# Kernel optimization log

Hardware: AMD Instinct MI355X
Metric: run time of the kernel (lower is better)

## Reference

```python
import jax, jax.numpy as jnp
import numpy as np

EPS = 1e-5  # nn.BatchNorm2d default eps
K = 3       # number of adjacency subsets


def setup_inputs() -> dict:
    key = jax.random.key(0)
    ks = jax.random.split(key, 8)
    N, C, T, V = 64, 64, 256, 25
    Cout = 64
    x = jax.random.normal(ks[0], (N, C, T, V), dtype=jnp.float32)
    A = jax.random.uniform(ks[1], (K, V, V), dtype=jnp.float32) * 0.1  # normalized-ish adjacency
    PA = jnp.ones((K, V, V), dtype=jnp.float32)  # torch.ones_like(A) init
    Wc = jax.random.normal(ks[2], (K * Cout, C), dtype=jnp.float32) * 0.05  # 1x1 conv weight
    bc = jax.random.normal(ks[3], (K * Cout,), dtype=jnp.float32) * 0.01
    gamma = 0.5 + jax.random.uniform(ks[4], (Cout,), dtype=jnp.float32)
    beta = jax.random.normal(ks[5], (Cout,), dtype=jnp.float32) * 0.1
    mean = jax.random.normal(ks[6], (Cout,), dtype=jnp.float32) * 0.1
    var = 0.5 + jax.random.uniform(ks[7], (Cout,), dtype=jnp.float32)
    return {"x": x, "A": A, "PA": PA, "Wc": Wc, "bc": bc,
            "gamma": gamma, "beta": beta, "mean": mean, "var": var}


def reference(x, A, PA, Wc, bc, gamma, beta, mean, var):
    # x: (n, c, t, v). in_channels == out_channels -> residual is identity.
    n, c, t, v = x.shape
    res = x
    Aeff = A * PA  # (k, v, w)
    # 1x1 conv: (n,c,t,v) x (o,c) -> (n,o,t,v), o = K*Cout
    y = jnp.einsum('nctv,oc->notv', x, Wc) + bc[None, :, None, None]
    cout = y.shape[1] // K
    y = y.reshape(n, K, cout, t, v)
    # per-subset graph aggregation: (n,k,c,t,v) x (k,v,w) -> (n,c,t,w)
    z = jnp.einsum('nkctv,kvw->nctw', y, Aeff)
    # BatchNorm2d (eval mode) over channel dim
    inv = jax.lax.rsqrt(var + EPS)
    bn = (z - mean[None, :, None, None]) * (gamma * inv)[None, :, None, None] + beta[None, :, None, None]
    return jax.nn.relu(bn + res)
```

## Files before the change

### kernel.cpp

```cpp
#include <hip/hip_runtime.h>
#include <hip/hip_bf16.h>

typedef __attribute__((ext_vector_type(8))) short short8;
typedef __attribute__((ext_vector_type(4))) float floatx4;

#define TT 8
#define XS_PITCH 264
#define KCP 200

__device__ __forceinline__ float bf2f(unsigned short u) {
    unsigned int xx = ((unsigned int)u) << 16;
    return __uint_as_float(xx);
}
__device__ __forceinline__ unsigned short f2bf(float f) {
    unsigned int xx = __float_as_uint(f);
    unsigned int r = (xx + 0x7fffu + ((xx >> 16) & 1u)) >> 16;
    return (unsigned short)r;
}

__global__ __launch_bounds__(512) void gcn_fused(
    const float* __restrict__ x,  const float* __restrict__ A,
    const float* __restrict__ PA, const float* __restrict__ Wc,
    const float* __restrict__ bc, const float* __restrict__ gamma_,
    const float* __restrict__ beta_, const float* __restrict__ mean_,
    const float* __restrict__ var_, float* __restrict__ out)
{
#if defined(__gfx950__)
    __shared__ __align__(16) unsigned short Xs[64 * XS_PITCH];
    __shared__ __align__(16) unsigned short AsL[96 * 32];
    __shared__ __align__(16) unsigned short XAs[32 * KCP];
    __shared__ float colsumL[96];
    __shared__ float sL[64], b2L[64], bcL[192];

    const int tid = threadIdx.x;
    const int n  = blockIdx.x >> 5;
    const int t0 = (blockIdx.x & 31) * TT;

    const float* xn = x + (size_t)n * 64 * 256 * 25;
    for (int idx = tid; idx < 64 * TT * 32; idx += 512) {
        int c = idx >> 8, r = idx & 255;
        int t = r >> 5, v = r & 31;
        float val = 0.f;
        if (v < 25) val = xn[(c * 256 + t0 + t) * 25 + v];
        Xs[c * XS_PITCH + r] = f2bf(val);
    }
    for (int idx = tid; idx < 96 * 32; idx += 512) {
        int kw = idx >> 5, v = idx & 31;
        int k = kw >> 5, w = kw & 31;
        unsigned short val = 0;
        if (w < 25 && v < 25) {
            int ai = (k * 25 + v) * 25 + w;
            val = f2bf(A[ai] * PA[ai]);
        }
        AsL[kw * 32 + v] = val;
    }
    if (tid < 96) {
        int k = tid >> 5, w = tid & 31;
        float s = 0.f;
        if (w < 25)
            for (int v = 0; v < 25; ++v) {
                int ai = (k * 25 + v) * 25 + w;
                s += A[ai] * PA[ai];
            }
        colsumL[tid] = s;
    }
    if (tid < 64) {
        float sc = gamma_[tid] * rsqrtf(var_[tid] + 1e-5f);
        sL[tid]  = sc;
        b2L[tid] = beta_[tid] - mean_[tid] * sc;
    }
    if (tid < 192) bcL[tid] = bc[tid];
    __syncthreads();

    const int wave = tid >> 6, lane = tid & 63;
    const int l15 = lane & 15, quad = lane >> 4;

    const int ntA = wave & 3, wmA = wave >> 2;
    short8 aA[3];
#pragma unroll
    for (int ii = 0; ii < 3; ++ii) {
        int mt = wmA + 2 * ii;
        aA[ii] = *(const short8*)&AsL[(mt * 16 + l15) * 32 + quad * 8];
    }

    const int cot = wave & 3, wt = wave >> 2;
    union U8 { short8 v; unsigned short s[8]; };
    short8 wf[6];
#pragma unroll
    for (int ks = 0; ks < 6; ++ks) {
        int k = ks >> 1;
        int co = cot * 16 + l15;
        int cpart = (ks & 1) * 32 + quad * 8;
        const float* wp = &Wc[(k * 64 + co) * 64 + cpart];
        U8 u;
#pragma unroll
        for (int j = 0; j < 8; ++j) u.s[j] = f2bf(wp[j]);
        wf[ks] = u.v;
    }

    for (int t = 0; t < TT; ++t) {
        short8 xb = *(const short8*)&Xs[(ntA * 16 + l15) * XS_PITCH + t * 32 + quad * 8];
        floatx4 fr[3];
#pragma unroll
        for (int ii = 0; ii < 3; ++ii) {
            floatx4 z0 = {0.f, 0.f, 0.f, 0.f};
            fr[ii] = __builtin_amdgcn_mfma_f32_16x16x32_bf16(aA[ii], xb, z0, 0, 0, 0);
        }
        __syncthreads();
#pragma unroll
        for (int ii = 0; ii < 3; ++ii) {
            int mt = wmA + 2 * ii;
#pragma unroll
            for (int r = 0; r < 4; ++r) {
                int kw = mt * 16 + quad * 4 + r;
                int w = kw & 31, k = kw >> 5;
                XAs[w * KCP + k * 64 + ntA * 16 + l15] = f2bf(fr[ii][r]);
            }
        }
        __syncthreads();

        floatx4 zacc = {0.f, 0.f, 0.f, 0.f};
        const unsigned short* xr = &XAs[(wt * 16 + l15) * KCP];
#pragma unroll
        for (int ks = 0; ks < 6; ++ks) {
            short8 bfr = *(const short8*)&xr[ks * 32 + quad * 8];
            zacc = __builtin_amdgcn_mfma_f32_16x16x32_bf16(wf[ks], bfr, zacc, 0, 0, 0);
        }

        int w = wt * 16 + l15;
        if (w < 25) {
            float cs0 = colsumL[w], cs1 = colsumL[32 + w], cs2 = colsumL[64 + w];
#pragma unroll
            for (int r = 0; r < 4; ++r) {
                int co = cot * 16 + quad * 4 + r;
                float bterm = bcL[co] * cs0 + bcL[64 + co] * cs1 + bcL[128 + co] * cs2;
                float xres = bf2f(Xs[co * XS_PITCH + t * 32 + w]);
                float val = sL[co] * (zacc[r] + bterm) + b2L[co] + xres;
                out[((size_t)(n * 64 + co) * 256 + t0 + t) * 25 + w] = fmaxf(val, 0.f);
            }
        }
    }
#else
    (void)x; (void)A; (void)PA; (void)Wc; (void)bc;
    (void)gamma_; (void)beta_; (void)mean_; (void)var_; (void)out;
#endif
}

extern "C" void kernel_launch(void* const* d_in, const int* in_sizes, int n_in,
                              void* d_out, int out_size, void* d_ws, size_t ws_size,
                              hipStream_t stream) {
    (void)in_sizes; (void)n_in; (void)d_ws; (void)ws_size; (void)out_size;
    gcn_fused<<<dim3(64 * 32), dim3(512), 0, stream>>>(
        (const float*)d_in[0],
        (const float*)d_in[1],
        (const float*)d_in[2],
        (const float*)d_in[3],
        (const float*)d_in[4],
        (const float*)d_in[5],
        (const float*)d_in[6],
        (const float*)d_in[7],
        (const float*)d_in[8],
        (float*)d_out);
}
```

Before: 304.8 us.

## Vectorize global loads/stores via LDS staging and double-buffer aggregation scratch

The input tile is now loaded with float4 reads of the contiguous (t,v) span per channel, with the v-padding zero-filled separately. Outputs are kept in registers across all time steps, staged transposed in LDS, and written back as coalesced float4 stores instead of scattered scalar stores. The intermediate XA buffer is double-buffered so one barrier per time step can be dropped. Adjacency fragments are built directly from global memory instead of through LDS, and occupancy is hinted with launch_bounds(512,4), which raises register pressure from the held output values.

```diff
diff --git a/kernel.cpp b/kernel.cpp
--- a/kernel.cpp
+++ b/kernel.cpp
@@ -1,5 +1,4 @@
 #include <hip/hip_runtime.h>
-#include <hip/hip_bf16.h>
 
 typedef __attribute__((ext_vector_type(8))) short short8;
 typedef __attribute__((ext_vector_type(4))) float floatx4;
@@ -7,6 +6,8 @@
 #define TT 8
 #define XS_PITCH 264
 #define KCP 200
+
+#define SMEM_BYTES 61056
 
 __device__ __forceinline__ float bf2f(unsigned short u) {
     unsigned int xx = ((unsigned int)u) << 16;
@@ -18,7 +19,7 @@
     return (unsigned short)r;
 }
 
-__global__ __launch_bounds__(512) void gcn_fused(
+__global__ __launch_bounds__(512, 4) void gcn_fused(
     const float* __restrict__ x,  const float* __restrict__ A,
     const float* __restrict__ PA, const float* __restrict__ Wc,
     const float* __restrict__ bc, const float* __restrict__ gamma_,
@@ -26,33 +27,36 @@
     const float* __restrict__ var_, float* __restrict__ out)
 {
 #if defined(__gfx950__)
-    __shared__ __align__(16) unsigned short Xs[64 * XS_PITCH];
-    __shared__ __align__(16) unsigned short AsL[96 * 32];
-    __shared__ __align__(16) unsigned short XAs[32 * KCP];
-    __shared__ float colsumL[96];
-    __shared__ float sL[64], b2L[64], bcL[192];
+    __shared__ __align__(16) unsigned char smem[SMEM_BYTES];
+    unsigned short* Xs  = (unsigned short*)smem;
+    unsigned short* XA0 = (unsigned short*)(smem + 33792);
+    unsigned short* XA1 = (unsigned short*)(smem + 46592);
+    float* colsumL = (float*)(smem + 59392);
+    float* sL      = (float*)(smem + 59776);
+    float* b2L     = (float*)(smem + 60032);
+    float* bcL     = (float*)(smem + 60288);
+    float* OutT    = (float*)smem;
 
     const int tid = threadIdx.x;
     const int n  = blockIdx.x >> 5;
     const int t0 = (blockIdx.x & 31) * TT;
 
-    const float* xn = x + (size_t)n * 64 * 256 * 25;
-    for (int idx = tid; idx < 64 * TT * 32; idx += 512) {
-        int c = idx >> 8, r = idx & 255;
-        int t = r >> 5, v = r & 31;
-        float val = 0.f;
-        if (v < 25) val = xn[(c * 256 + t0 + t) * 25 + v];
-        Xs[c * XS_PITCH + r] = f2bf(val);
-    }
-    for (int idx = tid; idx < 96 * 32; idx += 512) {
-        int kw = idx >> 5, v = idx & 31;
-        int k = kw >> 5, w = kw & 31;
-        unsigned short val = 0;
-        if (w < 25 && v < 25) {
-            int ai = (k * 25 + v) * 25 + w;
-            val = f2bf(A[ai] * PA[ai]);
-        }
-        AsL[kw * 32 + v] = val;
+    const float* xblk = x + (size_t)n * 409600 + t0 * 25;
+    for (int idx = tid; idx < 3200; idx += 512) {
+        int c = idx / 50, j4 = idx - c * 50;
+        float4 val = *(const float4*)(xblk + c * 6400 + j4 * 4);
+        int flat = j4 * 4;
+#pragma unroll
+        for (int e = 0; e < 4; ++e) {
+            int f = flat + e;
+            int t = f / 25, v = f - t * 25;
+            Xs[c * XS_PITCH + t * 32 + v] = f2bf(((const float*)&val)[e]);
+        }
+    }
+    for (int idx = tid; idx < 64 * TT * 7; idx += 512) {
+        int c = idx / 56, r = idx - c * 56;
+        int t = r / 7, v = 25 + (r - t * 7);
+        Xs[c * XS_PITCH + t * 32 + v] = 0;
     }
     if (tid < 96) {
         int k = tid >> 5, w = tid & 31;
@@ -70,21 +74,33 @@
         b2L[tid] = beta_[tid] - mean_[tid] * sc;
     }
     if (tid < 192) bcL[tid] = bc[tid];
-    __syncthreads();
 
     const int wave = tid >> 6, lane = tid & 63;
     const int l15 = lane & 15, quad = lane >> 4;
 
     const int ntA = wave & 3, wmA = wave >> 2;
+    union U8 { short8 v; unsigned short s[8]; };
     short8 aA[3];
 #pragma unroll
     for (int ii = 0; ii < 3; ++ii) {
         int mt = wmA + 2 * ii;
-        aA[ii] = *(const short8*)&AsL[(mt * 16 + l15) * 32 + quad * 8];
+        int kw = mt * 16 + l15;
+        int k = kw >> 5, w = kw & 31;
+        U8 u;
+#pragma unroll
+        for (int j = 0; j < 8; ++j) {
+            int v2 = quad * 8 + j;
+            float a = 0.f;
+            if (w < 25 && v2 < 25) {
+                int ai = (k * 25 + v2) * 25 + w;
+                a = A[ai] * PA[ai];
+            }
+            u.s[j] = f2bf(a);
+        }
+        aA[ii] = u.v;
     }
 
     const int cot = wave & 3, wt = wave >> 2;
-    union U8 { short8 v; unsigned short s[8]; };
     short8 wf[6];
 #pragma unroll
     for (int ks = 0; ks < 6; ++ks) {
@@ -98,7 +114,14 @@
         wf[ks] = u.v;
     }
 
+    __syncthreads();
+
+    const int w = wt * 16 + l15;
+    float vals[TT][4];
+
+#pragma unroll
     for (int t = 0; t < TT; ++t) {
+        unsigned short* XAw = (t & 1) ? XA1 : XA0;
         short8 xb = *(const short8*)&Xs[(ntA * 16 + l15) * XS_PITCH + t * 32 + quad * 8];
         floatx4 fr[3];
 #pragma unroll
@@ -106,39 +129,53 @@
             floatx4 z0 = {0.f, 0.f, 0.f, 0.f};
             fr[ii] = __builtin_amdgcn_mfma_f32_16x16x32_bf16(aA[ii], xb, z0, 0, 0, 0);
         }
-        __syncthreads();
 #pragma unroll
         for (int ii = 0; ii < 3; ++ii) {
             int mt = wmA + 2 * ii;
 #pragma unroll
             for (int r = 0; r < 4; ++r) {
                 int kw = mt * 16 + quad * 4 + r;
-                int w = kw & 31, k = kw >> 5;
-                XAs[w * KCP + k * 64 + ntA * 16 + l15] = f2bf(fr[ii][r]);
+                int ww = kw & 31, k = kw >> 5;
+                XAw[ww * KCP + k * 64 + ntA * 16 + l15] = f2bf(fr[ii][r]);
             }
         }
         __syncthreads();
 
         floatx4 zacc = {0.f, 0.f, 0.f, 0.f};
-        const unsigned short* xr = &XAs[(wt * 16 + l15) * KCP];
+        const unsigned short* xr = &XAw[(wt * 16 + l15) * KCP];
 #pragma unroll
         for (int ks = 0; ks < 6; ++ks) {
             short8 bfr = *(const short8*)&xr[ks * 32 + quad * 8];
             zacc = __builtin_amdgcn_mfma_f32_16x16x32_bf16(wf[ks], bfr, zacc, 0, 0, 0);
         }
 
-        int w = wt * 16 + l15;
-        if (w < 25) {
-            float cs0 = colsumL[w], cs1 = colsumL[32 + w], cs2 = colsumL[64 + w];
+        float cs0 = colsumL[w], cs1 = colsumL[32 + w], cs2 = colsumL[64 + w];
+#pragma unroll
+        for (int r = 0; r < 4; ++r) {
+            int co = cot * 16 + quad * 4 + r;
+            float bterm = bcL[co] * cs0 + bcL[64 + co] * cs1 + bcL[128 + co] * cs2;
+            float xres = bf2f(Xs[co * XS_PITCH + t * 32 + w]);
+            vals[t][r] = fmaxf(sL[co] * (zacc[r] + bterm) + b2L[co] + xres, 0.f);
+        }
+    }
+
+    __syncthreads();
+    if (w < 25) {
+#pragma unroll
+        for (int t = 0; t < TT; ++t)
 #pragma unroll
             for (int r = 0; r < 4; ++r) {
                 int co = cot * 16 + quad * 4 + r;
-                float bterm = bcL[co] * cs0 + bcL[64 + co] * cs1 + bcL[128 + co] * cs2;
-                float xres = bf2f(Xs[co * XS_PITCH + t * 32 + w]);
-                float val = sL[co] * (zacc[r] + bterm) + b2L[co] + xres;
-                out[((size_t)(n * 64 + co) * 256 + t0 + t) * 25 + w] = fmaxf(val, 0.f);
-            }
-        }
+                OutT[co * 200 + t * 25 + w] = vals[t][r];
+            }
+    }
+    __syncthreads();
+
+    float* oblk = out + (size_t)n * 409600 + t0 * 25;
+    for (int idx = tid; idx < 3200; idx += 512) {
+        int co = idx / 50, j4 = idx - co * 50;
+        float4 vv = *(const float4*)&OutT[co * 200 + j4 * 4];
+        *(float4*)(oblk + co * 6400 + j4 * 4) = vv;
     }
 #else
     (void)x; (void)A; (void)PA; (void)Wc; (void)bc;
```

After: 411.8 us. 35.1% more time.

## Shrink time tile to two steps per block and parallelize waves across them

Applied to the files above, without the earlier changes.

Each block now handles 2 time steps instead of 8, giving 4x more blocks. The wave-to-tile mapping is reorganized so all 8 waves work on both steps at once using a double-buffered XA region, which removes the per-step sync loop. LDS per block drops, so more blocks can be resident per CU, and the column sums are now taken from the bf16-rounded A in shared memory. The trade-off is that A/PA/W/BN setup is redone per block 4x more often, and each row's global load covers only 50 contiguous floats.

```diff
diff --git a/kernel.cpp b/kernel.cpp
--- a/kernel.cpp
+++ b/kernel.cpp
@@ -1,11 +1,10 @@
 #include <hip/hip_runtime.h>
-#include <hip/hip_bf16.h>
 
 typedef __attribute__((ext_vector_type(8))) short short8;
 typedef __attribute__((ext_vector_type(4))) float floatx4;
 
-#define TT 8
-#define XS_PITCH 264
+#define XSP 72
+#define ASP 32
 #define KCP 200
 
 __device__ __forceinline__ float bf2f(unsigned short u) {
@@ -26,43 +25,40 @@
     const float* __restrict__ var_, float* __restrict__ out)
 {
 #if defined(__gfx950__)
-    __shared__ __align__(16) unsigned short Xs[64 * XS_PITCH];
-    __shared__ __align__(16) unsigned short AsL[96 * 32];
-    __shared__ __align__(16) unsigned short XAs[32 * KCP];
+    __shared__ __align__(16) unsigned short Xs[64 * XSP];
+    __shared__ __align__(16) unsigned short AsL[96 * ASP];
+    __shared__ __align__(16) unsigned short XA[2 * 32 * KCP];
     __shared__ float colsumL[96];
     __shared__ float sL[64], b2L[64], bcL[192];
 
-    const int tid = threadIdx.x;
-    const int n  = blockIdx.x >> 5;
-    const int t0 = (blockIdx.x & 31) * TT;
+    const int tid  = threadIdx.x;
+    const int n    = blockIdx.x >> 7;
+    const int t0   = (blockIdx.x & 127) * 2;
+    const int wave = tid >> 6, lane = tid & 63;
+    const int l15  = lane & 15, quad = lane >> 4;
 
-    const float* xn = x + (size_t)n * 64 * 256 * 25;
-    for (int idx = tid; idx < 64 * TT * 32; idx += 512) {
-        int c = idx >> 8, r = idx & 255;
-        int t = r >> 5, v = r & 31;
+    const float* xblk = x + (size_t)n * 409600 + t0 * 25;
+
+#pragma unroll
+    for (int i = 0; i < 8; ++i) {
+        int idx = tid + i * 512;
+        int c = idx >> 6, rem = idx & 63;
+        int t = rem >> 5, v = rem & 31;
         float val = 0.f;
-        if (v < 25) val = xn[(c * 256 + t0 + t) * 25 + v];
-        Xs[c * XS_PITCH + r] = f2bf(val);
+        if (v < 25) val = xblk[c * 6400 + t * 25 + v];
+        Xs[c * XSP + t * 32 + v] = f2bf(val);
     }
-    for (int idx = tid; idx < 96 * 32; idx += 512) {
+#pragma unroll
+    for (int i = 0; i < 6; ++i) {
+        int idx = tid + i * 512;
         int kw = idx >> 5, v = idx & 31;
-        int k = kw >> 5, w = kw & 31;
-        unsigned short val = 0;
+        int ks = kw >> 5, w = kw & 31;
+        float a = 0.f;
         if (w < 25 && v < 25) {
-            int ai = (k * 25 + v) * 25 + w;
-            val = f2bf(A[ai] * PA[ai]);
+            int ai = (ks * 25 + v) * 25 + w;
+            a = A[ai] * PA[ai];
         }
-        AsL[kw * 32 + v] = val;
-    }
-    if (tid < 96) {
-        int k = tid >> 5, w = tid & 31;
-        float s = 0.f;
-        if (w < 25)
-            for (int v = 0; v < 25; ++v) {
-                int ai = (k * 25 + v) * 25 + w;
-                s += A[ai] * PA[ai];
-            }
-        colsumL[tid] = s;
+        AsL[kw * ASP + v] = f2bf(a);
     }
     if (tid < 64) {
         float sc = gamma_[tid] * rsqrtf(var_[tid] + 1e-5f);
@@ -70,20 +66,8 @@
         b2L[tid] = beta_[tid] - mean_[tid] * sc;
     }
     if (tid < 192) bcL[tid] = bc[tid];
-    __syncthreads();
 
-    const int wave = tid >> 6, lane = tid & 63;
-    const int l15 = lane & 15, quad = lane >> 4;
-
-    const int ntA = wave & 3, wmA = wave >> 2;
-    short8 aA[3];
-#pragma unroll
-    for (int ii = 0; ii < 3; ++ii) {
-        int mt = wmA + 2 * ii;
-        aA[ii] = *(const short8*)&AsL[(mt * 16 + l15) * 32 + quad * 8];
-    }
-
-    const int cot = wave & 3, wt = wave >> 2;
+    const int tB = wave & 1, cot = wave >> 1;
     union U8 { short8 v; unsigned short s[8]; };
     short8 wf[6];
 #pragma unroll
@@ -98,35 +82,56 @@
         wf[ks] = u.v;
     }
 
-    for (int t = 0; t < TT; ++t) {
-        short8 xb = *(const short8*)&Xs[(ntA * 16 + l15) * XS_PITCH + t * 32 + quad * 8];
-        floatx4 fr[3];
+    __syncthreads();
+
+    const int tA  = tB;
+    const int nt0 = cot & 1;
+    const int mt0 = cot >> 1;
+
+    short8 aA[3], xb[2];
 #pragma unroll
-        for (int ii = 0; ii < 3; ++ii) {
+    for (int m = 0; m < 3; ++m)
+        aA[m] = *(const short8*)&AsL[((mt0 + 2 * m) * 16 + l15) * ASP + quad * 8];
+#pragma unroll
+    for (int h = 0; h < 2; ++h)
+        xb[h] = *(const short8*)&Xs[((nt0 + 2 * h) * 16 + l15) * XSP + tA * 32 + quad * 8];
+
+    unsigned short* xaw = &XA[tA * 32 * KCP];
+#pragma unroll
+    for (int h = 0; h < 2; ++h) {
+        int ntc = (nt0 + 2 * h) * 16 + l15;
+#pragma unroll
+        for (int m = 0; m < 3; ++m) {
             floatx4 z0 = {0.f, 0.f, 0.f, 0.f};
-            fr[ii] = __builtin_amdgcn_mfma_f32_16x16x32_bf16(aA[ii], xb, z0, 0, 0, 0);
-        }
-        __syncthreads();
-#pragma unroll
-        for (int ii = 0; ii < 3; ++ii) {
-            int mt = wmA + 2 * ii;
+            floatx4 d = __builtin_amdgcn_mfma_f32_16x16x32_bf16(aA[m], xb[h], z0, 0, 0, 0);
+            int mt = mt0 + 2 * m;
 #pragma unroll
             for (int r = 0; r < 4; ++r) {
                 int kw = mt * 16 + quad * 4 + r;
-                int w = kw & 31, k = kw >> 5;
-                XAs[w * KCP + k * 64 + ntA * 16 + l15] = f2bf(fr[ii][r]);
+                int ww = kw & 31, ks = kw >> 5;
+                xaw[ww * KCP + ks * 64 + ntc] = f2bf(d[r]);
             }
         }
-        __syncthreads();
+    }
 
+    if (tid < 96) {
+        float s = 0.f;
+        for (int v = 0; v < 25; ++v) s += bf2f(AsL[tid * ASP + v]);
+        colsumL[tid] = s;
+    }
+
+    __syncthreads();
+
+    float* oblk = out + (size_t)n * 409600 + t0 * 25;
+#pragma unroll
+    for (int wt = 0; wt < 2; ++wt) {
+        const unsigned short* xr = &XA[tB * 32 * KCP + (wt * 16 + l15) * KCP];
         floatx4 zacc = {0.f, 0.f, 0.f, 0.f};
-        const unsigned short* xr = &XAs[(wt * 16 + l15) * KCP];
 #pragma unroll
         for (int ks = 0; ks < 6; ++ks) {
             short8 bfr = *(const short8*)&xr[ks * 32 + quad * 8];
             zacc = __builtin_amdgcn_mfma_f32_16x16x32_bf16(wf[ks], bfr, zacc, 0, 0, 0);
         }
-
         int w = wt * 16 + l15;
         if (w < 25) {
             float cs0 = colsumL[w], cs1 = colsumL[32 + w], cs2 = colsumL[64 + w];
@@ -134,9 +139,9 @@
             for (int r = 0; r < 4; ++r) {
                 int co = cot * 16 + quad * 4 + r;
                 float bterm = bcL[co] * cs0 + bcL[64 + co] * cs1 + bcL[128 + co] * cs2;
-                float xres = bf2f(Xs[co * XS_PITCH + t * 32 + w]);
+                float xres = bf2f(Xs[co * XSP + tB * 32 + w]);
                 float val = sL[co] * (zacc[r] + bterm) + b2L[co] + xres;
-                out[((size_t)(n * 64 + co) * 256 + t0 + t) * 25 + w] = fmaxf(val, 0.f);
+                oblk[co * 6400 + tB * 25 + w] = fmaxf(val, 0.f);
             }
         }
     }
@@ -150,7 +155,7 @@
                               void* d_out, int out_size, void* d_ws, size_t ws_size,
                               hipStream_t stream) {
     (void)in_sizes; (void)n_in; (void)d_ws; (void)ws_size; (void)out_size;
-    gcn_fused<<<dim3(64 * 32), dim3(512), 0, stream>>>(
+    gcn_fused<<<dim3(64 * 128), dim3(512), 0, stream>>>(
         (const float*)d_in[0],
         (const float*)d_in[1],
         (const float*)d_in[2],
```

After: 376.7 us. 1.24x slower.
